# Kernel optimization log

Hardware: AMD Instinct MI355X
Metric: run time of the kernel (lower is better)

The kernel has to match this reference:

```python
import jax, jax.numpy as jnp
import numpy as np

C_CURV = 1.0          # Poincare ball curvature c
EPS = 1e-15           # guard for norms / divisions
MAX_ATANH = 1.0 - 1e-5  # clamp artanh argument inside (-1, 1)


def _sqnorm(v):
    # squared norm along the manifold (channel) dim, axis=1
    return jnp.sum(v * v, axis=1, keepdims=True)


def _norm(v):
    return jnp.sqrt(jnp.clip(_sqnorm(v), EPS))


def _mobius_add(x, y, c):
    x2 = _sqnorm(x)
    y2 = _sqnorm(y)
    xy = jnp.sum(x * y, axis=1, keepdims=True)
    num = (1.0 + 2.0 * c * xy + c * y2) * x + (1.0 - c * x2) * y
    den = 1.0 + 2.0 * c * xy + (c * c) * x2 * y2
    return num / jnp.clip(den, EPS)


def _geodesic_midpoint(x, y, c):
    """expmap_x(0.5 * logmap_x(y)) on the Poincare ball, man_dim=1."""
    sc = jnp.sqrt(c)
    x2 = _sqnorm(x)
    lam = 2.0 / jnp.clip(1.0 - c * x2, EPS)  # conformal factor lambda_x
    # logmap_x(y)
    w = _mobius_add(-x, y, c)
    wn = _norm(w)
    v = (2.0 / (sc * lam)) * jnp.arctanh(jnp.clip(sc * wn, 0.0, MAX_ATANH)) * (w / wn)
    # half tangent vector
    v = 0.5 * v
    # expmap_x(v)
    vn = _norm(v)
    second = jnp.tanh(sc * lam * vn * 0.5) * (v / (sc * vn))
    return _mobius_add(x, second, c)


def setup_inputs() -> dict:
    key = jax.random.key(0)
    B, C, H, W = 8, 64, 128, 128
    n = jax.random.normal(key, (B, C, H, W), dtype=jnp.float32)
    # project strictly inside the unit ball along channel dim (valid Poincare points)
    nn_ = jnp.sqrt(jnp.clip(jnp.sum(n * n, axis=1, keepdims=True), EPS))
    x = 0.7 * n * jnp.tanh(nn_) / nn_
    return {"x": x}


def reference(x):
    c = C_CURV
    B, C_, H, W = x.shape
    Ho, Wo = 2 * H, 2 * W  # torch_like_size=True
    out = jnp.zeros((B, C_, Ho, Wo), dtype=x.dtype)
    # originals at even/even
    out = out.at[:, :, 0::2, 0::2].set(x)
    # horizontal midpoints: even rows, odd cols
    mid_h = _geodesic_midpoint(x[:, :, :, : W - 1], x[:, :, :, 1:], c)
    out = out.at[:, :, 0::2, 1:2 * (W - 1):2].set(mid_h)
    # vertical midpoints: odd rows, even cols
    mid_v = _geodesic_midpoint(x[:, :, : H - 1, :], x[:, :, 1:, :], c)
    out = out.at[:, :, 1:2 * (H - 1):2, 0::2].set(mid_v)
    # cell centers: bilinear via midpoints of horizontal midpoints
    x00 = x[:, :, : H - 1, : W - 1]
    x10 = x[:, :, : H - 1, 1:]
    x01 = x[:, :, 1:, : W - 1]
    x11 = x[:, :, 1:, 1:]
    a = _geodesic_midpoint(x00, x10, c)
    b = _geodesic_midpoint(x01, x11, c)
    center = _geodesic_midpoint(a, b, c)
    out = out.at[:, :, 1:2 * (H - 1):2, 1:2 * (W - 1):2].set(center)
    # torch-like size: duplicate last column/row
    out = out.at[:, :, :, -1].set(out[:, :, :, -2])
    out = out.at[:, :, -1, :].set(out[:, :, -2, :])
    return out
```

## Files before the change

### kernel.cpp

```cpp
#include <hip/hip_runtime.h>


#define EPSF   1e-15f
#define MAXAT  0.99999f

__device__ __forceinline__ void midcoef(float x2, float y2, float xy,
                                        float& A, float& B) {
    float alpha  = 1.0f - 2.0f * xy + y2;
    float beta   = 1.0f - x2;
    float den_w  = fmaxf(1.0f - 2.0f * xy + x2 * y2, EPSF);
    float inv_dw = 1.0f / den_w;
    float dxw = (beta * xy - alpha * x2) * inv_dw;
    float wn2 = (alpha * alpha * x2 - 2.0f * alpha * beta * xy + beta * beta * y2)
                * inv_dw * inv_dw;
    wn2 = fmaxf(wn2, EPSF);
    float wn = sqrtf(wn2);
    float a  = fminf(wn, MAXAT);
    float s  = a / (1.0f + sqrtf(fmaxf(1.0f - a * a, 0.0f)));
    float t  = s / wn;
    float xs = t * dxw;
    float s2 = t * t * wn2;
    float den     = fmaxf(1.0f + 2.0f * xs + x2 * s2, EPSF);
    float inv_den = 1.0f / den;
    float k = beta * t * inv_dw;
    A = ((1.0f + 2.0f * xs + s2) - k * alpha) * inv_den;
    B = (k * beta) * inv_den;
}

__global__ __launch_bounds__(512)
void hupsample_kernel(const float* __restrict__ x, float* __restrict__ out) {
    constexpr int C = 64, H = 128, W = 128;
    constexpr int CS = H * W;
    constexpr int CPS = C / 4;

    __shared__ float part[4][128][11];
    __shared__ float coef[128][9];

    const int w  = threadIdx.x;
    const int s  = threadIdx.y;
    const int h  = blockIdx.x;
    const int b  = blockIdx.y;
    const int wp = (w + 1 < W) ? (w + 1) : (W - 1);
    const int hp = (h + 1 < H) ? (h + 1) : (H - 1);

    const float* xb  = x + (size_t)b * C * CS + (size_t)(s * CPS) * CS;
    const float* p00 = xb + h  * W + w;
    const float* p10 = xb + h  * W + wp;
    const float* p01 = xb + hp * W + w;
    const float* p11 = xb + hp * W + wp;

    float g00 = 0.f, g10 = 0.f, g01 = 0.f, g11 = 0.f;
    float d0010 = 0.f, d0111 = 0.f, d0001 = 0.f;
    float d0011 = 0.f, d1001 = 0.f, d1011 = 0.f;
#pragma unroll 4
    for (int c = 0; c < CPS; ++c) {
        float v00 = p00[c * CS];
        float v10 = p10[c * CS];
        float v01 = p01[c * CS];
        float v11 = p11[c * CS];
        g00   += v00 * v00;  g10   += v10 * v10;
        g01   += v01 * v01;  g11   += v11 * v11;
        d0010 += v00 * v10;  d0111 += v01 * v11;
        d0001 += v00 * v01;  d0011 += v00 * v11;
        d1001 += v10 * v01;  d1011 += v10 * v11;
    }
    part[s][w][0] = g00;   part[s][w][1] = g10;
    part[s][w][2] = g01;   part[s][w][3] = g11;
    part[s][w][4] = d0010; part[s][w][5] = d0111;
    part[s][w][6] = d0001; part[s][w][7] = d0011;
    part[s][w][8] = d1001; part[s][w][9] = d1011;
    __syncthreads();

    if (s == 0) {
        float t0[10];
#pragma unroll
        for (int k = 0; k < 10; ++k)
            t0[k] = part[0][w][k] + part[1][w][k] + part[2][w][k] + part[3][w][k];
        float G00 = t0[0], G10 = t0[1], G01 = t0[2], G11 = t0[3];
        float D0010 = t0[4], D0111 = t0[5], D0001 = t0[6];
        float D0011 = t0[7], D1001 = t0[8], D1011 = t0[9];

        float Ah, Bh;  midcoef(G00, G10, D0010, Ah, Bh);
        float A2, B2;  midcoef(G01, G11, D0111, A2, B2);
        float Av, Bv;  midcoef(G00, G01, D0001, Av, Bv);

        float a2 = Ah * Ah * G00 + 2.0f * Ah * Bh * D0010 + Bh * Bh * G10;
        float b2 = A2 * A2 * G01 + 2.0f * A2 * B2 * D0111 + B2 * B2 * G11;
        float ab = Ah * A2 * D0001 + Ah * B2 * D0011
                 + Bh * A2 * D1001 + Bh * B2 * D1011;
        float A3, B3;  midcoef(a2, b2, ab, A3, B3);

        coef[w][0] = Ah;      coef[w][1] = Bh;
        coef[w][2] = Av;      coef[w][3] = Bv;
        coef[w][4] = A3 * Ah; coef[w][5] = A3 * Bh;
        coef[w][6] = B3 * A2; coef[w][7] = B3 * B2;
    }
    __syncthreads();

    const float Ah = coef[w][0], Bh = coef[w][1];
    const float Av = coef[w][2], Bv = coef[w][3];
    const float CA = coef[w][4], CB = coef[w][5];
    const float CC = coef[w][6], CD = coef[w][7];

    float* ob = out + (size_t)b * C * (4 * CS) + (size_t)(s * CPS) * (4 * CS);
    const size_t rbase = (size_t)(2 * h) * (2 * W) + (size_t)(2 * w);
#pragma unroll 4
    for (int c = 0; c < CPS; ++c) {
        float v00 = p00[c * CS];
        float v10 = p10[c * CS];
        float v01 = p01[c * CS];
        float v11 = p11[c * CS];
        float oh = Ah * v00 + Bh * v10;
        float ov = Av * v00 + Bv * v01;
        float oc = CA * v00 + CB * v10 + CC * v01 + CD * v11;
        size_t base = (size_t)c * (4 * CS) + rbase;
        *(float2*)(ob + base)         = make_float2(v00, oh);
        *(float2*)(ob + base + 2 * W) = make_float2(ov, oc);
    }
}

extern "C" void kernel_launch(void* const* d_in, const int* in_sizes, int n_in,
                              void* d_out, int out_size, void* d_ws, size_t ws_size,
                              hipStream_t stream) {
    const float* x = (const float*)d_in[0];
    float* out = (float*)d_out;
    dim3 grid(128, 8);
    dim3 block(128, 4);
    hipLaunchKernelGGL(hupsample_kernel, grid, block, 0, stream, x, out);
}
```

Before: 168.3 us.

## Split fused kernel into coefficient pass and channel-parallel apply pass

```diff
diff --git a/kernel.cpp b/kernel.cpp
--- a/kernel.cpp
+++ b/kernel.cpp
@@ -27,37 +27,37 @@
     B = (k * beta) * inv_den;
 }
 
+constexpr int Cc = 64, Hc = 128, Wc = 128;
+constexpr int CSc = Hc * Wc;
+constexpr int NCELL = 8 * Hc * Wc;
+
 __global__ __launch_bounds__(512)
-void hupsample_kernel(const float* __restrict__ x, float* __restrict__ out) {
-    constexpr int C = 64, H = 128, W = 128;
-    constexpr int CS = H * W;
-    constexpr int CPS = C / 4;
-
+void coef_kernel(const float* __restrict__ x, float* __restrict__ cof) {
+    constexpr int CPS = Cc / 4;
     __shared__ float part[4][128][11];
-    __shared__ float coef[128][9];
 
     const int w  = threadIdx.x;
     const int s  = threadIdx.y;
     const int h  = blockIdx.x;
     const int b  = blockIdx.y;
-    const int wp = (w + 1 < W) ? (w + 1) : (W - 1);
-    const int hp = (h + 1 < H) ? (h + 1) : (H - 1);
+    const int wp = (w + 1 < Wc) ? (w + 1) : (Wc - 1);
+    const int hp = (h + 1 < Hc) ? (h + 1) : (Hc - 1);
 
-    const float* xb  = x + (size_t)b * C * CS + (size_t)(s * CPS) * CS;
-    const float* p00 = xb + h  * W + w;
-    const float* p10 = xb + h  * W + wp;
-    const float* p01 = xb + hp * W + w;
-    const float* p11 = xb + hp * W + wp;
+    const float* xb  = x + (size_t)b * Cc * CSc + (size_t)(s * CPS) * CSc;
+    const float* p00 = xb + h  * Wc + w;
+    const float* p10 = xb + h  * Wc + wp;
+    const float* p01 = xb + hp * Wc + w;
+    const float* p11 = xb + hp * Wc + wp;
 
     float g00 = 0.f, g10 = 0.f, g01 = 0.f, g11 = 0.f;
     float d0010 = 0.f, d0111 = 0.f, d0001 = 0.f;
     float d0011 = 0.f, d1001 = 0.f, d1011 = 0.f;
 #pragma unroll 4
     for (int c = 0; c < CPS; ++c) {
-        float v00 = p00[c * CS];
-        float v10 = p10[c * CS];
-        float v01 = p01[c * CS];
-        float v11 = p11[c * CS];
+        float v00 = p00[c * CSc];
+        float v10 = p10[c * CSc];
+        float v01 = p01[c * CSc];
+        float v11 = p11[c * CSc];
         g00   += v00 * v00;  g10   += v10 * v10;
         g01   += v01 * v01;  g11   += v11 * v11;
         d0010 += v00 * v10;  d0111 += v01 * v11;
@@ -90,32 +90,47 @@
                  + Bh * A2 * D1001 + Bh * B2 * D1011;
         float A3, B3;  midcoef(a2, b2, ab, A3, B3);
 
-        coef[w][0] = Ah;      coef[w][1] = Bh;
-        coef[w][2] = Av;      coef[w][3] = Bv;
-        coef[w][4] = A3 * Ah; coef[w][5] = A3 * Bh;
-        coef[w][6] = B3 * A2; coef[w][7] = B3 * B2;
+        const size_t ci = (size_t)(b * Hc + h) * Wc + w;
+        cof[0 * NCELL + ci] = Ah;      cof[1 * NCELL + ci] = Bh;
+        cof[2 * NCELL + ci] = Av;      cof[3 * NCELL + ci] = Bv;
+        cof[4 * NCELL + ci] = A3 * Ah; cof[5 * NCELL + ci] = A3 * Bh;
+        cof[6 * NCELL + ci] = B3 * A2; cof[7 * NCELL + ci] = B3 * B2;
     }
-    __syncthreads();
+}
 
-    const float Ah = coef[w][0], Bh = coef[w][1];
-    const float Av = coef[w][2], Bv = coef[w][3];
-    const float CA = coef[w][4], CB = coef[w][5];
-    const float CC = coef[w][6], CD = coef[w][7];
+__global__ __launch_bounds__(128)
+void apply_kernel(const float* __restrict__ x, const float* __restrict__ cof,
+                  float* __restrict__ out) {
+    const int w  = threadIdx.x;
+    const int h  = blockIdx.x;
+    const int cg = blockIdx.y;
+    const int b  = blockIdx.z;
+    const int wp = (w + 1 < Wc) ? (w + 1) : (Wc - 1);
+    const int hp = (h + 1 < Hc) ? (h + 1) : (Hc - 1);
 
-    float* ob = out + (size_t)b * C * (4 * CS) + (size_t)(s * CPS) * (4 * CS);
-    const size_t rbase = (size_t)(2 * h) * (2 * W) + (size_t)(2 * w);
-#pragma unroll 4
-    for (int c = 0; c < CPS; ++c) {
-        float v00 = p00[c * CS];
-        float v10 = p10[c * CS];
-        float v01 = p01[c * CS];
-        float v11 = p11[c * CS];
+    const size_t ci = (size_t)(b * Hc + h) * Wc + w;
+    const float Ah = cof[0 * NCELL + ci], Bh = cof[1 * NCELL + ci];
+    const float Av = cof[2 * NCELL + ci], Bv = cof[3 * NCELL + ci];
+    const float CA = cof[4 * NCELL + ci], CB = cof[5 * NCELL + ci];
+    const float CC = cof[6 * NCELL + ci], CD = cof[7 * NCELL + ci];
+
+    const int c0 = cg * 4;
+    const float* xc = x + ((size_t)b * Cc + c0) * CSc;
+    float* ob = out + ((size_t)b * Cc + c0) * (4 * CSc)
+              + (size_t)(2 * h) * (2 * Wc) + (size_t)(2 * w);
+
+#pragma unroll
+    for (int c = 0; c < 4; ++c) {
+        float v00 = xc[c * CSc + h  * Wc + w];
+        float v10 = xc[c * CSc + h  * Wc + wp];
+        float v01 = xc[c * CSc + hp * Wc + w];
+        float v11 = xc[c * CSc + hp * Wc + wp];
         float oh = Ah * v00 + Bh * v10;
         float ov = Av * v00 + Bv * v01;
         float oc = CA * v00 + CB * v10 + CC * v01 + CD * v11;
-        size_t base = (size_t)c * (4 * CS) + rbase;
-        *(float2*)(ob + base)         = make_float2(v00, oh);
-        *(float2*)(ob + base + 2 * W) = make_float2(ov, oc);
+        float* o = ob + (size_t)c * (4 * CSc);
+        *(float2*)o             = make_float2(v00, oh);
+        *(float2*)(o + 2 * Wc)  = make_float2(ov, oc);
     }
 }
 
@@ -124,7 +139,13 @@
                               hipStream_t stream) {
     const float* x = (const float*)d_in[0];
     float* out = (float*)d_out;
-    dim3 grid(128, 8);
-    dim3 block(128, 4);
-    hipLaunchKernelGGL(hupsample_kernel, grid, block, 0, stream, x, out);
+    float* cof = (float*)d_ws;
+
+    dim3 gridA(128, 8);
+    dim3 blockA(128, 4);
+    hipLaunchKernelGGL(coef_kernel, gridA, blockA, 0, stream, x, cof);
+
+    dim3 gridB(128, 16, 8);
+    dim3 blockB(128);
+    hipLaunchKernelGGL(apply_kernel, gridB, blockB, 0, stream, x, cof, out);
 }
```

Result: no change. 167.3 us (-0.6%).
